# Optimization experiments

Measured on AMD Instinct MI355X. Metric: run time of the kernel, lower is better.

Reference implementation:

```python
import jax, jax.numpy as jnp
import numpy as np

N, E, D_IN, D_H, D_OUT = 100000, 1600000, 128, 128, 47
BN_EPS = 1e-5


def setup_inputs() -> dict:
    key = jax.random.key(0)
    ks = jax.random.split(key, 12)
    x = jax.random.normal(ks[0], (N, D_IN), dtype=jnp.float32)
    edge_index = jax.random.randint(ks[1], (2, E), 0, N, dtype=jnp.int64)
    s = 1.0 / np.sqrt(D_H)
    return {
        "x": x,
        "edge_index": edge_index,
        "W1": jax.random.normal(ks[2], (D_IN, D_H), dtype=jnp.float32) * s,
        "b1": jnp.zeros((D_H,), dtype=jnp.float32),
        "gamma": jax.random.uniform(ks[3], (D_H,), dtype=jnp.float32, minval=0.5, maxval=1.5),
        "beta": jax.random.normal(ks[4], (D_H,), dtype=jnp.float32) * 0.1,
        "mean": jax.random.normal(ks[5], (D_H,), dtype=jnp.float32) * 0.1,
        "var": jax.random.uniform(ks[6], (D_H,), dtype=jnp.float32, minval=0.5, maxval=1.5),
        "W2": jax.random.normal(ks[7], (D_H, D_H), dtype=jnp.float32) * s,
        "b2": jnp.zeros((D_H,), dtype=jnp.float32),
        "Wf": jax.random.normal(ks[8], (D_H, D_OUT), dtype=jnp.float32) * s,
        "bf": jnp.zeros((D_OUT,), dtype=jnp.float32),
    }


def gcn_conv(x, src, dst, W, b, n):
    # x' = x @ W, then symmetric-normalized aggregation with self-loops (PyG GCNConv).
    h = x @ W
    loops = jnp.arange(n, dtype=src.dtype)
    s = jnp.concatenate([src, loops])
    d = jnp.concatenate([dst, loops])
    deg = jax.ops.segment_sum(jnp.ones_like(d, dtype=h.dtype), d, num_segments=n)
    dinv = jnp.where(deg > 0, jax.lax.rsqrt(deg), 0.0)
    norm = dinv[s] * dinv[d]                      # [E+N]
    msg = h[s] * norm[:, None]                    # [E+N, D] gather
    out = jax.ops.segment_sum(msg, d, num_segments=n)  # scatter-add
    return out + b


def reference(x, edge_index, W1, b1, gamma, beta, mean, var, W2, b2, Wf, bf):
    n = x.shape[0]
    src, dst = edge_index[0], edge_index[1]
    # layer 1: GCNConv -> BatchNorm (eval) -> ReLU -> dropout (identity in eval)
    h1 = gcn_conv(x, src, dst, W1, b1, n)
    h1 = (h1 - mean) * jax.lax.rsqrt(var + BN_EPS) * gamma + beta
    h1 = jax.nn.relu(h1)
    # layer 2 (last conv, no BN/act)
    h2 = gcn_conv(h1, src, dst, W2, b2, n)
    # JumpingKnowledge max over layer outputs
    jk = jnp.maximum(h1, h2)
    logits = jk @ Wf + bf
    return jax.nn.log_softmax(logits, axis=1)
```

## Files before the change

### kernel.cpp

```cpp
#include <hip/hip_runtime.h>
#include <math.h>

#define DH 128
#define DOUT 47
#define BN_EPS 1e-5f

typedef __attribute__((ext_vector_type(8))) short short8;
typedef __attribute__((ext_vector_type(4))) float float4v;

__device__ __forceinline__ unsigned bf16_rne(float f) {
    unsigned u = __float_as_uint(f);
    return (u + 0x7fffu + ((u >> 16) & 1u)) >> 16;
}
__device__ __forceinline__ unsigned pack_bf2(float a, float b) {
    return (bf16_rne(a) & 0xffffu) | (bf16_rne(b) << 16);
}
__device__ __forceinline__ float2 unpack_bf2(unsigned u) {
    return make_float2(__uint_as_float(u << 16),
                       __uint_as_float(u & 0xffff0000u));
}


__global__ void zero_int_k(int* __restrict__ p, int n) {
    int i = blockIdx.x * 256 + threadIdx.x;
    if (i < n) p[i] = 0;
}

__global__ __launch_bounds__(256) void count_rank_k(const int* __restrict__ dst,
                                                    int* __restrict__ counts,
                                                    int* __restrict__ rank, int e) {
    int i0 = (blockIdx.x * 256 + threadIdx.x) * 4;
    if (i0 + 4 <= e) {
        int4 d4 = *(const int4*)(dst + i0);
        int4 r4;
        r4.x = atomicAdd(&counts[d4.x], 1);
        r4.y = atomicAdd(&counts[d4.y], 1);
        r4.z = atomicAdd(&counts[d4.z], 1);
        r4.w = atomicAdd(&counts[d4.w], 1);
        *(int4*)(rank + i0) = r4;
    } else {
        for (int i = i0; i < e; i++) rank[i] = atomicAdd(&counts[dst[i]], 1);
    }
}

__global__ __launch_bounds__(256) void scan1_k(const int* __restrict__ counts,
                                               int* __restrict__ offsets,
                                               int* __restrict__ blocksums, int n) {
    __shared__ int sd[256];
    int tid = threadIdx.x;
    int base = blockIdx.x * 1024 + tid * 4;
    int v0 = (base + 0 < n) ? ((counts[base + 0] + 7) & ~7) : 0;
    int v1 = (base + 1 < n) ? ((counts[base + 1] + 7) & ~7) : 0;
    int v2 = (base + 2 < n) ? ((counts[base + 2] + 7) & ~7) : 0;
    int v3 = (base + 3 < n) ? ((counts[base + 3] + 7) & ~7) : 0;
    int tsum = v0 + v1 + v2 + v3;
    sd[tid] = tsum;
    __syncthreads();
    for (int off = 1; off < 256; off <<= 1) {
        int x = (tid >= off) ? sd[tid - off] : 0;
        __syncthreads();
        sd[tid] += x;
        __syncthreads();
    }
    if (tid == 255) blocksums[blockIdx.x] = sd[255];
    int run = sd[tid] - tsum;
    if (base + 0 < n) offsets[base + 0] = run;  run += v0;
    if (base + 1 < n) offsets[base + 1] = run;  run += v1;
    if (base + 2 < n) offsets[base + 2] = run;  run += v2;
    if (base + 3 < n) offsets[base + 3] = run;
}

__global__ __launch_bounds__(128) void scan2_k(int* __restrict__ blocksums, int nb) {
    __shared__ int sd[128];
    int tid = threadIdx.x;
    int v = (tid < nb) ? blocksums[tid] : 0;
    sd[tid] = v;
    __syncthreads();
    for (int off = 1; off < 128; off <<= 1) {
        int x = (tid >= off) ? sd[tid - off] : 0;
        __syncthreads();
        sd[tid] += x;
        __syncthreads();
    }
    if (tid < nb) blocksums[tid] = sd[tid] - v;
}

__global__ void finalize_k(int* __restrict__ offsets,
                           float* __restrict__ dinv, const int* __restrict__ counts,
                           const int* __restrict__ blocksums,
                           int2* __restrict__ ew, int n) {
    int i = blockIdx.x * 256 + threadIdx.x;
    if (i >= n) return;
    int o = offsets[i] + blocksums[i >> 10];
    offsets[i] = o;
    int c = counts[i];
    dinv[i] = rsqrtf((float)(c + 1));
    int cP = (c + 7) & ~7;
    int2 z; z.x = 0; z.y = 0;
    for (int j = o + c; j < o + cP; ++j) ew[j] = z;
}

__global__ __launch_bounds__(256) void scatter_k(const int* __restrict__ src,
                                                 const int* __restrict__ dst,
                                                 const int* __restrict__ rank,
                                                 const int* __restrict__ offsets,
                                                 const float* __restrict__ dinv,
                                                 int2* __restrict__ ew, int e) {
    int i0 = (blockIdx.x * 256 + threadIdx.x) * 4;
    if (i0 + 4 <= e) {
        int4 s4 = *(const int4*)(src + i0);
        int4 d4 = *(const int4*)(dst + i0);
        int4 r4 = *(const int4*)(rank + i0);
        int sa[4] = {s4.x, s4.y, s4.z, s4.w};
        int da[4] = {d4.x, d4.y, d4.z, d4.w};
        int ra[4] = {r4.x, r4.y, r4.z, r4.w};
        int slot[4];
        float w[4];
#pragma unroll
        for (int k = 0; k < 4; k++) slot[k] = offsets[da[k]] + ra[k];
#pragma unroll
        for (int k = 0; k < 4; k++) w[k] = dinv[sa[k]] * dinv[da[k]];
#pragma unroll
        for (int k = 0; k < 4; k++) {
            int2 r; r.x = sa[k]; r.y = __float_as_int(w[k]);
            ew[slot[k]] = r;
        }
    } else {
        for (int i = i0; i < e; i++) {
            int s = src[i], d = dst[i];
            int2 r; r.x = s; r.y = __float_as_int(dinv[s] * dinv[d]);
            ew[offsets[d] + rank[i]] = r;
        }
    }
}

__global__ __launch_bounds__(256) void wprep_k(const float* __restrict__ W1,
                                               const float* __restrict__ W2,
                                               unsigned* __restrict__ W1b,
                                               unsigned* __restrict__ W2b) {
    const float* W = blockIdx.x ? W2 : W1;
    unsigned* Wb = blockIdx.x ? W2b : W1b;
    int tid = threadIdx.x;
    for (int p = tid; p < 128 * 32; p += 256) {
        int n = p >> 5;
        int k0 = (p & 31) << 2;
        float f0 = W[(size_t)(k0 + 0) * 128 + n];
        float f1 = W[(size_t)(k0 + 1) * 128 + n];
        float f2 = W[(size_t)(k0 + 2) * 128 + n];
        float f3 = W[(size_t)(k0 + 3) * 128 + n];
        uint2 v;
        v.x = pack_bf2(f0, f1);
        v.y = pack_bf2(f2, f3);
        *(uint2*)(Wb + (size_t)n * 64 + (k0 >> 1)) = v;
    }
}

__global__ __launch_bounds__(256) void gemm_mfma_k(const float* __restrict__ A,
                                                   const unsigned* __restrict__ Wb,
                                                   unsigned* __restrict__ Cb, int M) {
    __shared__ ushort Bl[128 * 136];
    int tid = threadIdx.x;
    {
        unsigned* Bu = (unsigned*)Bl;
        for (int q = tid; q < 128 * 16; q += 256) {
            int row = q >> 4;
            int c = (q & 15) << 2;
            uint4 v = *(const uint4*)(Wb + (size_t)row * 64 + c);
            *(uint4*)(Bu + (size_t)row * 68 + c) = v;
        }
    }
    __syncthreads();

    int lane = tid & 63;
    int wv = tid >> 6;
    int quad = lane >> 4;
    int l15 = lane & 15;
    int r0 = blockIdx.x * 64 + wv * 16;
    int mload = r0 + l15;
    if (mload > M - 1) mload = M - 1;
    const float* Ar = A + (size_t)mload * 128 + quad * 8;

    float4v acc[8];
#pragma unroll
    for (int t = 0; t < 8; t++) acc[t] = (float4v){0.f, 0.f, 0.f, 0.f};

    for (int kp = 0; kp < 4; ++kp) {
        float4 a0 = *(const float4*)(Ar + kp * 32);
        float4 a1 = *(const float4*)(Ar + kp * 32 + 4);
        float af[8] = {a0.x, a0.y, a0.z, a0.w, a1.x, a1.y, a1.z, a1.w};
        short8 hi, lo;
#pragma unroll
        for (int j = 0; j < 8; j++) {
            unsigned h = bf16_rne(af[j]);
            hi[j] = (short)h;
            float res = af[j] - __uint_as_float(h << 16);
            lo[j] = (short)bf16_rne(res);
        }
        int kb = kp * 32 + quad * 8;
#pragma unroll
        for (int nt = 0; nt < 8; nt++) {
            short8 b8 = *(const short8*)(&Bl[(size_t)(nt * 16 + l15) * 136 + kb]);
            acc[nt] = __builtin_amdgcn_mfma_f32_16x16x32_bf16(hi, b8, acc[nt], 0, 0, 0);
            acc[nt] = __builtin_amdgcn_mfma_f32_16x16x32_bf16(lo, b8, acc[nt], 0, 0, 0);
        }
    }

    ushort* Cu = (ushort*)Cb;
#pragma unroll
    for (int r = 0; r < 4; r++) {
        int row = r0 + quad * 4 + r;
        if (row < M) {
#pragma unroll
            for (int nt = 0; nt < 8; nt++) {
                Cu[(size_t)row * 128 + nt * 16 + l15] = (ushort)bf16_rne(acc[nt][r]);
            }
        }
    }
}

__device__ __forceinline__ float4 agg_core(const uint2* __restrict__ Hu2,
                                           const int2* __restrict__ ew,
                                           int start, int cnt, int node,
                                           int li, int half, float di) {
    float4 acc = make_float4(0.f, 0.f, 0.f, 0.f);
    int groups = ((cnt + 7) & ~7) >> 3;
    if (groups > 0) {
        const int2* p = ew + start + half;
        int2 r[4];
#pragma unroll
        for (int k = 0; k < 4; k++) r[k] = p[2 * k];
        for (int g = 0; g < groups; ++g) {
            uint2 gb[4];
#pragma unroll
            for (int k = 0; k < 4; k++)
                gb[k] = Hu2[(size_t)r[k].x * 32 + li];
            int2 rn[4];
            const int2* pn = p + 8 * (g + 1);
#pragma unroll
            for (int k = 0; k < 4; k++) rn[k] = pn[2 * k];
#pragma unroll
            for (int k = 0; k < 4; k++) {
                float w = __int_as_float(r[k].y);
                float2 f0 = unpack_bf2(gb[k].x);
                float2 f1 = unpack_bf2(gb[k].y);
                acc.x = fmaf(f0.x, w, acc.x);
                acc.y = fmaf(f0.y, w, acc.y);
                acc.z = fmaf(f1.x, w, acc.z);
                acc.w = fmaf(f1.y, w, acc.w);
            }
#pragma unroll
            for (int k = 0; k < 4; k++) r[k] = rn[k];
        }
    }
    acc.x += __shfl_xor(acc.x, 32);
    acc.y += __shfl_xor(acc.y, 32);
    acc.z += __shfl_xor(acc.z, 32);
    acc.w += __shfl_xor(acc.w, 32);
    uint2 sv = Hu2[(size_t)node * 32 + li];
    float ws = di * di;
    float2 s0 = unpack_bf2(sv.x);
    float2 s1 = unpack_bf2(sv.y);
    acc.x = fmaf(s0.x, ws, acc.x);
    acc.y = fmaf(s0.y, ws, acc.y);
    acc.z = fmaf(s1.x, ws, acc.z);
    acc.w = fmaf(s1.y, ws, acc.w);
    return acc;
}

__global__ __launch_bounds__(256) void agg1_k(
    const unsigned* __restrict__ H, const int2* __restrict__ ew,
    const int* __restrict__ offsets, const int* __restrict__ counts,
    const float* __restrict__ dinv, const float* __restrict__ b1,
    const float* __restrict__ gamma, const float* __restrict__ beta,
    const float* __restrict__ mean, const float* __restrict__ var,
    float* __restrict__ H1, int n) {
    int lane = threadIdx.x & 63;
    int li = lane & 31;
    int half = lane >> 5;
    int node = blockIdx.x * 4 + (threadIdx.x >> 6);
    if (node >= n) return;
    float4 acc = agg_core((const uint2*)H, ew, offsets[node], counts[node],
                          node, li, half, dinv[node]);
    if (half == 0) {
        int f0 = li * 4;
        float4 bb = *(const float4*)(b1 + f0);
        float4 mm = *(const float4*)(mean + f0);
        float4 vv = *(const float4*)(var + f0);
        float4 gg = *(const float4*)(gamma + f0);
        float4 be = *(const float4*)(beta + f0);
        float4 o;
        o.x = fmaxf((acc.x + bb.x - mm.x) * rsqrtf(vv.x + BN_EPS) * gg.x + be.x, 0.f);
        o.y = fmaxf((acc.y + bb.y - mm.y) * rsqrtf(vv.y + BN_EPS) * gg.y + be.y, 0.f);
        o.z = fmaxf((acc.z + bb.z - mm.z) * rsqrtf(vv.z + BN_EPS) * gg.z + be.z, 0.f);
        o.w = fmaxf((acc.w + bb.w - mm.w) * rsqrtf(vv.w + BN_EPS) * gg.w + be.w, 0.f);
        *(float4*)(H1 + (size_t)node * 128 + f0) = o;
    }
}

__global__ __launch_bounds__(256) void agg2_k(
    const unsigned* __restrict__ H, const int2* __restrict__ ew,
    const int* __restrict__ offsets, const int* __restrict__ counts,
    const float* __restrict__ dinv, const float* __restrict__ b2,
    float* __restrict__ H1JK, int n) {
    int lane = threadIdx.x & 63;
    int li = lane & 31;
    int half = lane >> 5;
    int node = blockIdx.x * 4 + (threadIdx.x >> 6);
    if (node >= n) return;
    float4 acc = agg_core((const uint2*)H, ew, offsets[node], counts[node],
                          node, li, half, dinv[node]);
    if (half == 0) {
        int f0 = li * 4;
        float4 bb = *(const float4*)(b2 + f0);
        float4* p = (float4*)(H1JK + (size_t)node * 128 + f0);
        float4 h1v = *p;
        float4 o;
        o.x = fmaxf(h1v.x, acc.x + bb.x);
        o.y = fmaxf(h1v.y, acc.y + bb.y);
        o.z = fmaxf(h1v.z, acc.z + bb.z);
        o.w = fmaxf(h1v.w, acc.w + bb.w);
        *p = o;
    }
}

__global__ __launch_bounds__(256) void head_k(const float* __restrict__ JK,
                                              const float* __restrict__ Wf,
                                              const float* __restrict__ bf,
                                              float* __restrict__ out, int n) {
    __shared__ __align__(16) float Bs[48 * 132];
    __shared__ __align__(16) float As[64 * 36];
    int tid = threadIdx.x;
    for (int p = tid; p < 47 * 32; p += 256) {
        int c = p >> 5;
        int k0 = (p & 31) << 2;
        float4 v;
        v.x = Wf[(size_t)(k0 + 0) * DOUT + c];
        v.y = Wf[(size_t)(k0 + 1) * DOUT + c];
        v.z = Wf[(size_t)(k0 + 2) * DOUT + c];
        v.w = Wf[(size_t)(k0 + 3) * DOUT + c];
        *(float4*)(&Bs[c * 132 + k0]) = v;
    }
    int tx = tid & 15;
    int ty = tid >> 4;
    int node0 = blockIdx.x * 64;

    float acc[4][3];
#pragma unroll
    for (int i = 0; i < 4; i++)
#pragma unroll
        for (int j = 0; j < 3; j++) acc[i][j] = 0.f;

    for (int kk = 0; kk < 128; kk += 32) {
        __syncthreads();
        for (int l = tid; l < 512; l += 256) {
            int r = l >> 3;
            int c4 = (l & 7) << 2;
            int row = node0 + r;
            float4 v = make_float4(0.f, 0.f, 0.f, 0.f);
            if (row < n) v = *(const float4*)(JK + (size_t)row * 128 + kk + c4);
            *(float4*)(&As[r * 36 + c4]) = v;
        }
        __syncthreads();
#pragma unroll
        for (int k4 = 0; k4 < 32; k4 += 4) {
            float4 a0 = *(const float4*)(&As[(ty * 4 + 0) * 36 + k4]);
            float4 a1 = *(const float4*)(&As[(ty * 4 + 1) * 36 + k4]);
            float4 a2 = *(const float4*)(&As[(ty * 4 + 2) * 36 + k4]);
            float4 a3 = *(const float4*)(&As[(ty * 4 + 3) * 36 + k4]);
            float4 b0 = *(const float4*)(&Bs[(tx * 3 + 0) * 132 + kk + k4]);
            float4 b1 = *(const float4*)(&Bs[(tx * 3 + 1) * 132 + kk + k4]);
            float4 b2 = *(const float4*)(&Bs[(tx * 3 + 2) * 132 + kk + k4]);
#define DOT_ROW(i, a)                                                        \
            acc[i][0] = fmaf(a.x, b0.x, acc[i][0]);                          \
            acc[i][0] = fmaf(a.y, b0.y, acc[i][0]);                          \
            acc[i][0] = fmaf(a.z, b0.z, acc[i][0]);                          \
            acc[i][0] = fmaf(a.w, b0.w, acc[i][0]);                          \
            acc[i][1] = fmaf(a.x, b1.x, acc[i][1]);                          \
            acc[i][1] = fmaf(a.y, b1.y, acc[i][1]);                          \
            acc[i][1] = fmaf(a.z, b1.z, acc[i][1]);                          \
            acc[i][1] = fmaf(a.w, b1.w, acc[i][1]);                          \
            acc[i][2] = fmaf(a.x, b2.x, acc[i][2]);                          \
            acc[i][2] = fmaf(a.y, b2.y, acc[i][2]);                          \
            acc[i][2] = fmaf(a.z, b2.z, acc[i][2]);                          \
            acc[i][2] = fmaf(a.w, b2.w, acc[i][2]);
            DOT_ROW(0, a0)
            DOT_ROW(1, a1)
            DOT_ROW(2, a2)
            DOT_ROW(3, a3)
#undef DOT_ROW
        }
    }

    float bfv[3];
#pragma unroll
    for (int j = 0; j < 3; j++) {
        int c = tx * 3 + j;
        bfv[j] = (c < DOUT) ? bf[c] : 0.f;
    }
#pragma unroll
    for (int i = 0; i < 4; i++) {
        int node = node0 + ty * 4 + i;
        float l0 = acc[i][0] + bfv[0];
        float l1 = acc[i][1] + bfv[1];
        float l2 = acc[i][2] + bfv[2];
        bool v2ok = (tx * 3 + 2) < DOUT;
        float m = fmaxf(l0, l1);
        if (v2ok) m = fmaxf(m, l2);
        for (int off = 8; off >= 1; off >>= 1) m = fmaxf(m, __shfl_xor(m, off));
        float s = expf(l0 - m) + expf(l1 - m) + (v2ok ? expf(l2 - m) : 0.f);
        for (int off = 8; off >= 1; off >>= 1) s += __shfl_xor(s, off);
        float ls = m + logf(s);
        if (node < n) {
            float* o = out + (size_t)node * DOUT + tx * 3;
            o[0] = l0 - ls;
            o[1] = l1 - ls;
            if (v2ok) o[2] = l2 - ls;
        }
    }
}

extern "C" void kernel_launch(void* const* d_in, const int* in_sizes, int n_in,
                              void* d_out, int out_size, void* d_ws, size_t ws_size,
                              hipStream_t stream) {
    const float* x     = (const float*)d_in[0];
    const int*   ei    = (const int*)d_in[1];
    const float* W1    = (const float*)d_in[2];
    const float* b1    = (const float*)d_in[3];
    const float* gamma = (const float*)d_in[4];
    const float* beta  = (const float*)d_in[5];
    const float* mean  = (const float*)d_in[6];
    const float* var   = (const float*)d_in[7];
    const float* W2    = (const float*)d_in[8];
    const float* b2    = (const float*)d_in[9];
    const float* Wf    = (const float*)d_in[10];
    const float* bf    = (const float*)d_in[11];
    float* out = (float*)d_out;

    int N_ = in_sizes[0] / 128;
    int E_ = in_sizes[1] / 2;
    const int* src = ei;
    const int* dst = ei + E_;

    char* ws = (char*)d_ws;
    unsigned* bufA = (unsigned*)ws; ws += (size_t)N_ * 64 * 4;
    float* h1      = (float*)ws;  ws += (size_t)N_ * 128 * 4;
    int*   counts  = (int*)ws;    ws += (size_t)N_ * 4;
    int*   offsets = (int*)ws;    ws += (size_t)N_ * 4;
    float* dinv    = (float*)ws;  ws += (size_t)N_ * 4;
    int*   rank    = (int*)ws;    ws += (size_t)E_ * 4;
    int2*  ew      = (int2*)ws;   ws += ((size_t)E_ + 7 * (size_t)N_ + 64) * 8;
    int*   bsums   = (int*)ws;    ws += 1024 * 4;
    unsigned* W1b  = (unsigned*)ws; ws += 128 * 64 * 4;
    unsigned* W2b  = (unsigned*)ws; ws += 128 * 64 * 4;

    int nb = (N_ + 1023) / 1024;
    int gemmBlocks = (N_ + 63) / 64;
    int edgeBlocks = (E_ + 1023) / 1024;

    zero_int_k<<<(N_ + 255) / 256, 256, 0, stream>>>(counts, N_);
    wprep_k<<<2, 256, 0, stream>>>(W1, W2, W1b, W2b);
    count_rank_k<<<edgeBlocks, 256, 0, stream>>>(dst, counts, rank, E_);
    scan1_k<<<nb, 256, 0, stream>>>(counts, offsets, bsums, N_);
    scan2_k<<<1, 128, 0, stream>>>(bsums, nb);
    finalize_k<<<(N_ + 255) / 256, 256, 0, stream>>>(offsets, dinv,
                                                     counts, bsums, ew, N_);
    scatter_k<<<edgeBlocks, 256, 0, stream>>>(src, dst, rank, offsets, dinv, ew, E_);

    gemm_mfma_k<<<gemmBlocks, 256, 0, stream>>>(x, W1b, bufA, N_);
    agg1_k<<<(N_ + 3) / 4, 256, 0, stream>>>(bufA, ew, offsets, counts, dinv,
                                             b1, gamma, beta, mean, var, h1, N_);
    gemm_mfma_k<<<gemmBlocks, 256, 0, stream>>>(h1, W2b, bufA, N_);
    agg2_k<<<(N_ + 3) / 4, 256, 0, stream>>>(bufA, ew, offsets, counts, dinv,
                                             b2, h1, N_);
    head_k<<<(N_ + 63) / 64, 256, 0, stream>>>(h1, Wf, bf, out, N_);
}
```

Baseline: 470.8 us.

## Store layer-1 activations and JK buffer in bf16 and add bf16-input GEMM

Switches the intermediate h1/JK buffer from fp32 to packed bf16, so agg1 writes, agg2 reads and writes, and head reads half as many bytes. A new gemm_bf16_k consumes the bf16 activations directly with a single MFMA per k-step, replacing the hi/lo split fp32 GEMM used for layer 2. The trade-off is lower precision: h1 is rounded to bf16 before the layer-2 GEMM and before the JK max and final head, which may loosen accuracy against the fp32 reference.

```diff
diff --git a/kernel.cpp b/kernel.cpp
--- a/kernel.cpp
+++ b/kernel.cpp
@@ -218,6 +218,63 @@
     }
 }
 
+__global__ __launch_bounds__(256) void gemm_bf16_k(const unsigned* __restrict__ Ab,
+                                                   const unsigned* __restrict__ Wb,
+                                                   unsigned* __restrict__ Cb, int M) {
+    __shared__ ushort Bl[128 * 136];
+    int tid = threadIdx.x;
+    {
+        unsigned* Bu = (unsigned*)Bl;
+        for (int q = tid; q < 128 * 16; q += 256) {
+            int row = q >> 4;
+            int c = (q & 15) << 2;
+            uint4 v = *(const uint4*)(Wb + (size_t)row * 64 + c);
+            *(uint4*)(Bu + (size_t)row * 68 + c) = v;
+        }
+    }
+    __syncthreads();
+
+    int lane = tid & 63;
+    int wv = tid >> 6;
+    int quad = lane >> 4;
+    int l15 = lane & 15;
+    int r0 = blockIdx.x * 64 + wv * 16;
+    int mload = r0 + l15;
+    if (mload > M - 1) mload = M - 1;
+    const unsigned* Ar = Ab + (size_t)mload * 64 + quad * 4;
+
+    float4v acc[8];
+#pragma unroll
+    for (int t = 0; t < 8; t++) acc[t] = (float4v){0.f, 0.f, 0.f, 0.f};
+
+    for (int kp = 0; kp < 4; ++kp) {
+        uint4 a4 = *(const uint4*)(Ar + kp * 16);
+        short8 av;
+        av[0] = (short)(a4.x & 0xffff); av[1] = (short)(a4.x >> 16);
+        av[2] = (short)(a4.y & 0xffff); av[3] = (short)(a4.y >> 16);
+        av[4] = (short)(a4.z & 0xffff); av[5] = (short)(a4.z >> 16);
+        av[6] = (short)(a4.w & 0xffff); av[7] = (short)(a4.w >> 16);
+        int kb = kp * 32 + quad * 8;
+#pragma unroll
+        for (int nt = 0; nt < 8; nt++) {
+            short8 b8 = *(const short8*)(&Bl[(size_t)(nt * 16 + l15) * 136 + kb]);
+            acc[nt] = __builtin_amdgcn_mfma_f32_16x16x32_bf16(av, b8, acc[nt], 0, 0, 0);
+        }
+    }
+
+    ushort* Cu = (ushort*)Cb;
+#pragma unroll
+    for (int r = 0; r < 4; r++) {
+        int row = r0 + quad * 4 + r;
+        if (row < M) {
+#pragma unroll
+            for (int nt = 0; nt < 8; nt++) {
+                Cu[(size_t)row * 128 + nt * 16 + l15] = (ushort)bf16_rne(acc[nt][r]);
+            }
+        }
+    }
+}
+
 __device__ __forceinline__ float4 agg_core(const uint2* __restrict__ Hu2,
                                            const int2* __restrict__ ew,
                                            int start, int cnt, int node,
@@ -273,7 +330,7 @@
     const float* __restrict__ dinv, const float* __restrict__ b1,
     const float* __restrict__ gamma, const float* __restrict__ beta,
     const float* __restrict__ mean, const float* __restrict__ var,
-    float* __restrict__ H1, int n) {
+    unsigned* __restrict__ H1b, int n) {
     int lane = threadIdx.x & 63;
     int li = lane & 31;
     int half = lane >> 5;
@@ -293,7 +350,10 @@
         o.y = fmaxf((acc.y + bb.y - mm.y) * rsqrtf(vv.y + BN_EPS) * gg.y + be.y, 0.f);
         o.z = fmaxf((acc.z + bb.z - mm.z) * rsqrtf(vv.z + BN_EPS) * gg.z + be.z, 0.f);
         o.w = fmaxf((acc.w + bb.w - mm.w) * rsqrtf(vv.w + BN_EPS) * gg.w + be.w, 0.f);
-        *(float4*)(H1 + (size_t)node * 128 + f0) = o;
+        uint2 pk;
+        pk.x = pack_bf2(o.x, o.y);
+        pk.y = pack_bf2(o.z, o.w);
+        *(uint2*)(H1b + (size_t)node * 64 + li * 2) = pk;
     }
 }
 
@@ -301,7 +361,7 @@
     const unsigned* __restrict__ H, const int2* __restrict__ ew,
     const int* __restrict__ offsets, const int* __restrict__ counts,
     const float* __restrict__ dinv, const float* __restrict__ b2,
-    float* __restrict__ H1JK, int n) {
+    unsigned* __restrict__ H1b, int n) {
     int lane = threadIdx.x & 63;
     int li = lane & 31;
     int half = lane >> 5;
@@ -312,18 +372,23 @@
     if (half == 0) {
         int f0 = li * 4;
         float4 bb = *(const float4*)(b2 + f0);
-        float4* p = (float4*)(H1JK + (size_t)node * 128 + f0);
-        float4 h1v = *p;
+        uint2* p = (uint2*)(H1b + (size_t)node * 64 + li * 2);
+        uint2 hv = *p;
+        float2 ha = unpack_bf2(hv.x);
+        float2 hb = unpack_bf2(hv.y);
         float4 o;
-        o.x = fmaxf(h1v.x, acc.x + bb.x);
-        o.y = fmaxf(h1v.y, acc.y + bb.y);
-        o.z = fmaxf(h1v.z, acc.z + bb.z);
-        o.w = fmaxf(h1v.w, acc.w + bb.w);
-        *p = o;
-    }
-}
-
-__global__ __launch_bounds__(256) void head_k(const float* __restrict__ JK,
+        o.x = fmaxf(ha.x, acc.x + bb.x);
+        o.y = fmaxf(ha.y, acc.y + bb.y);
+        o.z = fmaxf(hb.x, acc.z + bb.z);
+        o.w = fmaxf(hb.y, acc.w + bb.w);
+        uint2 pk;
+        pk.x = pack_bf2(o.x, o.y);
+        pk.y = pack_bf2(o.z, o.w);
+        *p = pk;
+    }
+}
+
+__global__ __launch_bounds__(256) void head_k(const unsigned* __restrict__ JKb,
                                               const float* __restrict__ Wf,
                                               const float* __restrict__ bf,
                                               float* __restrict__ out, int n) {
@@ -357,7 +422,12 @@
             int c4 = (l & 7) << 2;
             int row = node0 + r;
             float4 v = make_float4(0.f, 0.f, 0.f, 0.f);
-            if (row < n) v = *(const float4*)(JK + (size_t)row * 128 + kk + c4);
+            if (row < n) {
+                uint2 u = *(const uint2*)(JKb + (size_t)row * 64 + ((kk + c4) >> 1));
+                float2 f0 = unpack_bf2(u.x);
+                float2 f1 = unpack_bf2(u.y);
+                v = make_float4(f0.x, f0.y, f1.x, f1.y);
+            }
             *(float4*)(&As[r * 36 + c4]) = v;
         }
         __syncthreads();
@@ -443,7 +513,7 @@
 
     char* ws = (char*)d_ws;
     unsigned* bufA = (unsigned*)ws; ws += (size_t)N_ * 64 * 4;
-    float* h1      = (float*)ws;  ws += (size_t)N_ * 128 * 4;
+    unsigned* h1b  = (unsigned*)ws; ws += (size_t)N_ * 64 * 4;
     int*   counts  = (int*)ws;    ws += (size_t)N_ * 4;
     int*   offsets = (int*)ws;    ws += (size_t)N_ * 4;
     float* dinv    = (float*)ws;  ws += (size_t)N_ * 4;
@@ -468,9 +538,9 @@
 
     gemm_mfma_k<<<gemmBlocks, 256, 0, stream>>>(x, W1b, bufA, N_);
     agg1_k<<<(N_ + 3) / 4, 256, 0, stream>>>(bufA, ew, offsets, counts, dinv,
-                                             b1, gamma, beta, mean, var, h1, N_);
-    gemm_mfma_k<<<gemmBlocks, 256, 0, stream>>>(h1, W2b, bufA, N_);
+                                             b1, gamma, beta, mean, var, h1b, N_);
+    gemm_bf16_k<<<gemmBlocks, 256, 0, stream>>>(h1b, W2b, bufA, N_);
     agg2_k<<<(N_ + 3) / 4, 256, 0, stream>>>(bufA, ew, offsets, counts, dinv,
-                                             b2, h1, N_);
-    head_k<<<(N_ + 63) / 64, 256, 0, stream>>>(h1, Wf, bf, out, N_);
-}
+                                             b2, h1b, N_);
+    head_k<<<(N_ + 63) / 64, 256, 0, stream>>>(h1b, Wf, bf, out, N_);
+}
```

Result: faster. 461.3 us (-2.0%).
